# Optimization experiments

Measured on AMD Instinct MI355X. Metric: run time of the kernel, lower is better.

Reference implementation:

```python
import jax, jax.numpy as jnp
import numpy as np

B, NORM_NC, LABEL_NC, H, W, SL = 8, 256, 19, 64, 64, 512
EPS = 1e-5


def _conv5(x, w, b):
    # 5x5 'same' conv, NCHW / OIHW
    y = jax.lax.conv_general_dilated(x, w, (1, 1), [(2, 2), (2, 2)],
                                     dimension_numbers=('NCHW', 'OIHW', 'NCHW'))
    return y + b[None, :, None, None]


def _instance_norm(x):
    # InstanceNorm2d(affine=False): per-sample, per-channel over HxW, biased var
    m = x.mean(axis=(2, 3), keepdims=True)
    v = x.var(axis=(2, 3), keepdims=True)
    return (x - m) / jnp.sqrt(v + EPS)


def setup_inputs() -> dict:
    key = jax.random.key(0)
    ks = jax.random.split(key, 12)
    # one-hot semantic segmentation map (what segmap.bool() assumes in practice)
    labels = jax.random.randint(ks[0], (B, H, W), 0, LABEL_NC)
    segmap = jax.nn.one_hot(labels, LABEL_NC, axis=1, dtype=jnp.float32)  # [B,19,H,W]
    s = 0.02
    return {
        'x': jax.random.normal(ks[1], (B, NORM_NC, H, W), jnp.float32),
        'segmap': segmap,
        'style_codes': jax.random.normal(ks[2], (B, LABEL_NC, SL), jnp.float32),
        'fc_w': jax.random.normal(ks[3], (LABEL_NC, SL, SL), jnp.float32) * s,
        'fc_b': jnp.zeros((LABEL_NC, SL), jnp.float32),
        'conv_gamma_w': jax.random.normal(ks[4], (NORM_NC, SL, 5, 5), jnp.float32) * s,
        'conv_gamma_b': jnp.zeros((NORM_NC,), jnp.float32),
        'conv_beta_w': jax.random.normal(ks[5], (NORM_NC, SL, 5, 5), jnp.float32) * s,
        'conv_beta_b': jnp.zeros((NORM_NC,), jnp.float32),
        'spade_shared_w': jax.random.normal(ks[6], (512, LABEL_NC, 5, 5), jnp.float32) * s,
        'spade_shared_b': jnp.zeros((512,), jnp.float32),
        'spade_gamma_w': jax.random.normal(ks[7], (NORM_NC, 512, 5, 5), jnp.float32) * s,
        'spade_gamma_b': jnp.zeros((NORM_NC,), jnp.float32),
        'spade_beta_w': jax.random.normal(ks[8], (NORM_NC, 512, 5, 5), jnp.float32) * s,
        'spade_beta_b': jnp.zeros((NORM_NC,), jnp.float32),
        'blending_gamma': jnp.zeros((1,), jnp.float32),
        'blending_beta': jnp.zeros((1,), jnp.float32),
    }


def reference(x, segmap, style_codes, fc_w, fc_b,
              conv_gamma_w, conv_gamma_b, conv_beta_w, conv_beta_b,
              spade_shared_w, spade_shared_b,
              spade_gamma_w, spade_gamma_b, spade_beta_w, spade_beta_b,
              blending_gamma, blending_beta):
    normalized = _instance_norm(x)
    # F.interpolate(segmap, size=x.shape[2:], mode='nearest') is identity here
    # (segmap already has x's spatial size).
    mask = segmap > 0  # segmap.bool(): [B,J,H,W]
    J = mask.shape[1]

    # per-class style MLP: mu[b,j] = relu(fc_mu_j(style_codes[b,j]))
    mu = jax.nn.relu(jnp.einsum('bjd,jed->bje', style_codes, fc_w) + fc_b)  # [B,J,SL]

    # for overlapping masks; pixels with no class stay zero.
    last_idx = (J - 1) - jnp.argmax(mask[:, ::-1], axis=1)  # [B,H,W] last true j
    any_m = mask.any(axis=1)                                 # [B,H,W]
    mu_sel = mu[jnp.arange(mu.shape[0])[:, None, None], last_idx]  # [B,H,W,SL]
    middle_avg = jnp.where(any_m[..., None], mu_sel, 0.0).transpose(0, 3, 1, 2)

    gamma_avg = _conv5(middle_avg, conv_gamma_w, conv_gamma_b)
    beta_avg = _conv5(middle_avg, conv_beta_w, conv_beta_b)

    actv = jax.nn.relu(_conv5(segmap, spade_shared_w, spade_shared_b))
    gamma_spade = _conv5(actv, spade_gamma_w, spade_gamma_b)
    beta_spade = _conv5(actv, spade_beta_w, spade_beta_b)

    ga = jax.nn.sigmoid(blending_gamma)  # shape (1,) broadcasts
    ba = jax.nn.sigmoid(blending_beta)
    gamma_final = ga * gamma_avg + (1 - ga) * gamma_spade
    beta_final = ba * beta_avg + (1 - ba) * beta_spade
    return normalized * (1 + gamma_final) + beta_final
```

## Files before the change

### kernel.cpp

```cpp
#include <hip/hip_runtime.h>
#include <hip/hip_bf16.h>
#include <stdint.h>

typedef __attribute__((__ext_vector_type__(8))) __bf16 bf16x8;
typedef __attribute__((__ext_vector_type__(2))) __bf16 bf16x2;
typedef __attribute__((__ext_vector_type__(4))) float  f32x4;
typedef __attribute__((__ext_vector_type__(8))) int    v8i;

#define SCALE_A_DW 0x77777777
#define SCALE_B_DW 0x79797979

__device__ __forceinline__ void gl_lds16(const void* g, void* l) {
  __builtin_amdgcn_global_load_lds(
      (__attribute__((address_space(1))) void*)(uintptr_t)g,
      (__attribute__((address_space(3))) void*)(unsigned)(uintptr_t)l,
      16, 0, 0);
}

__global__ __launch_bounds__(256) void k_prep(
    const float* __restrict__ x, float* __restrict__ stats,
    const float* __restrict__ seg, int* __restrict__ labels,
    const float* __restrict__ cgw, const float* __restrict__ cbw,
    float* __restrict__ wpa,
    const float* __restrict__ ssw, __bf16* __restrict__ wspb,
    __bf16* __restrict__ Aav) {
  __shared__ __align__(16) char smem[16*401*4];
  int blk = blockIdx.x;
  if (blk < 2048) {
    int bc = blk;
    const float4* p = (const float4*)(x + (size_t)bc * 4096);
    float s = 0.f, ss = 0.f;
    for (int i = threadIdx.x; i < 1024; i += 256) {
      float4 v = p[i];
      s  += v.x + v.y + v.z + v.w;
      ss += v.x*v.x + v.y*v.y + v.z*v.z + v.w*v.w;
    }
    #pragma unroll
    for (int o = 32; o > 0; o >>= 1) { s += __shfl_down(s, o); ss += __shfl_down(ss, o); }
    float* sh = (float*)smem;
    int wv = threadIdx.x >> 6;
    if ((threadIdx.x & 63) == 0) { sh[wv] = s; sh[4 + wv] = ss; }
    __syncthreads();
    if (threadIdx.x == 0) {
      float S = sh[0]+sh[1]+sh[2]+sh[3], SS = sh[4]+sh[5]+sh[6]+sh[7];
      float m = S * (1.f/4096.f);
      float var = SS * (1.f/4096.f) - m*m;
      stats[bc] = m;
      stats[2048 + bc] = rsqrtf(var + 1e-5f);
    }
  } else if (blk < 2176) {
    int idx = (blk - 2048)*256 + threadIdx.x;
    int b = idx >> 12, pix = idx & 4095;
    const float* p = seg + (size_t)b*19*4096 + pix;
    int lab = -1;
    for (int j = 0; j < 19; ++j) if (p[(size_t)j*4096] > 0.f) lab = j;
    labels[idx] = lab;
  } else if (blk < 3200) {
    int bid = blk - 2176;
    float* s = (float*)smem;
    int n0 = (bid & 31) * 16, c0 = (bid >> 5) * 16;
    for (int i = threadIdx.x; i < 6400; i += 256) {
      int nn = i / 400, qq = i % 400;
      int n = n0 + nn;
      const float* src = (n < 256) ? cgw + (size_t)n*12800 : cbw + (size_t)(n-256)*12800;
      s[nn*401 + qq] = src[c0*25 + qq];
    }
    __syncthreads();
    for (int i = threadIdx.x; i < 6400; i += 256) {
      int nn = i & 15, rest = i >> 4;
      int k5 = rest % 25, cc = rest / 25;
      wpa[((size_t)k5*512 + c0 + cc)*512 + n0 + nn] = s[nn*401 + cc*25 + k5];
    }
  } else if (blk < 4200) {
    int idx = (blk - 3200)*256 + threadIdx.x;
    int o = idx & 511, k5 = (idx >> 9) % 25, j = idx / 12800;
    wspb[idx] = (j < 19) ? (__bf16)ssw[((size_t)o*19 + j)*25 + k5] : (__bf16)0.f;
  } else {
    ((unsigned*)(Aav + 3800ull*512))[threadIdx.x] = 0;
  }
}

__global__ __launch_bounds__(512) void k_mu(const float* __restrict__ sc,
                                            const float* __restrict__ fcw,
                                            const float* __restrict__ fcb,
                                            float* __restrict__ mu) {
  int b = blockIdx.x / 19, j = blockIdx.x % 19;
  __shared__ float s[512];
  s[threadIdx.x] = sc[(b*19 + j)*512 + threadIdx.x];
  __syncthreads();
  int e = threadIdx.x;
  const float4* w4 = (const float4*)(fcw + ((size_t)(j*512 + e))*512);
  const float4* s4 = (const float4*)s;
  float acc = 0.f;
  for (int d = 0; d < 128; ++d) {
    float4 w = w4[d], v = s4[d];
    acc += w.x*v.x + w.y*v.y + w.z*v.z + w.w*v.w;
  }
  acc += fcb[j*512 + e];
  mu[(b*19 + j)*512 + e] = fmaxf(acc, 0.f);
}

__global__ __launch_bounds__(256) void k_pack_spade(
    const float* __restrict__ g, const float* __restrict__ bt,
    uint8_t* __restrict__ wq) {
  int n = blockIdx.x;
  const float* src = (n < 256) ? g + (size_t)n*12800 : bt + (size_t)(n-256)*12800;
  __shared__ float s[12800];
  for (int i = threadIdx.x; i < 12800; i += 256) s[i] = src[i];
  __syncthreads();
  int t = threadIdx.x;
  for (int k5 = 0; k5 < 25; ++k5) {
    float w0 = s[(2*t)*25 + k5] * 64.f, w1 = s[(2*t+1)*25 + k5] * 64.f;
    int pk = __builtin_amdgcn_cvt_pk_fp8_f32(w0, w1, 0, false);
    *(unsigned short*)(wq + ((size_t)k5*512 + n)*512 + 2*t) = (unsigned short)pk;
  }
}

__global__ __launch_bounds__(512) void k_A_avg(const float* __restrict__ mu,
                                               const float* __restrict__ wpa,
                                               __bf16* __restrict__ A) {
  int b = blockIdx.x / 25, k5 = blockIdx.x % 25;
  int n = threadIdx.x;
  const float* wp = wpa + (size_t)k5*262144 + n;
  const float* mub = mu + b*19*512;
  float acc[19];
  #pragma unroll
  for (int j = 0; j < 19; ++j) acc[j] = 0.f;
  for (int c = 0; c < 512; ++c) {
    float w = wp[(size_t)c*512];
    #pragma unroll
    for (int j = 0; j < 19; ++j) acc[j] += mub[j*512 + c] * w;
  }
  #pragma unroll
  for (int j = 0; j < 19; ++j)
    A[((size_t)((b*19 + j)*25 + k5))*512 + n] = (__bf16)acc[j];
}

__global__ void k_actv(const int* __restrict__ labels, const __bf16* __restrict__ wsp,
                       const float* __restrict__ ssb, uint8_t* __restrict__ actv) {
  int b = blockIdx.x / 68, hp = blockIdx.x % 68;
  int t = threadIdx.x;
  size_t rowbase = ((size_t)b*68 + hp)*68;
  if (hp < 2 || hp >= 66) {
    unsigned* dp = (unsigned*)(actv + rowbase*512);
    for (int i = t; i < 8704; i += 256) dp[i] = 0;
    return;
  }
  int h = hp - 2;
  __shared__ int lab[5*68];
  for (int i = t; i < 5*68; i += 256) {
    int dh = i / 68, xx = i % 68;
    int hh = h + dh - 2, ww = xx - 2;
    int l = 19;
    if (hh >= 0 && hh < 64 && ww >= 0 && ww < 64) {
      int l0 = labels[b*4096 + hh*64 + ww];
      if (l0 >= 0) l = l0;
    }
    lab[i] = l;
  }
  {
    unsigned* dp = (unsigned*)(actv + rowbase*512);
    dp[t] = 0; dp[66*128 + t] = 0;
  }
  __syncthreads();
  float bs0 = ssb[2*t], bs1 = ssb[2*t + 1];
  for (int w = 0; w < 64; ++w) {
    float a0 = bs0, a1 = bs1;
    #pragma unroll
    for (int tap = 0; tap < 25; ++tap) {
      int l = lab[(tap/5)*68 + w + (tap%5)];
      bf16x2 v = *(const bf16x2*)(wsp + (size_t)(l*25 + tap)*512 + 2*t);
      a0 += (float)v[0]; a1 += (float)v[1];
    }
    a0 = fmaxf(a0, 0.f) * 256.f;
    a1 = fmaxf(a1, 0.f) * 256.f;
    int pk = __builtin_amdgcn_cvt_pk_fp8_f32(a0, a1, 0, false);
    *(unsigned short*)(actv + (rowbase + 2 + w)*512 + 2*t) = (unsigned short)pk;
  }
}

__global__ __launch_bounds__(512) void k_conv(
    const uint8_t* __restrict__ actv, const uint8_t* __restrict__ wq,
    const float* __restrict__ sgb, const float* __restrict__ sbb,
    __bf16* __restrict__ gbs) {
  __shared__ __align__(16) uint8_t ldsA[2][32768];
  __shared__ __align__(16) uint8_t ldsB[2][32768];
  const int tid = threadIdx.x, wv = tid >> 6, lane = tid & 63;
  const int l15 = lane & 15, q = lane >> 4;
  const int m0 = blockIdx.x * 256, n0 = blockIdx.y * 256;
  const int b = m0 >> 12;

  int aoff[4], boff[4], ldst[4];
  #pragma unroll
  for (int i = 0; i < 4; ++i) {
    int p = i*512 + tid;
    int r = p >> 3, pc = p & 7;
    int cl = pc ^ (r & 7);
    int pix = (m0 + r) & 4095;
    int h = pix >> 6, w = pix & 63;
    aoff[i] = ((b*68 + h)*68 + w)*512 + cl*16;
    boff[i] = (n0 + r)*512 + cl*16;
    ldst[i] = i*8192 + wv*1024;
  }

  const int wm = (wv >> 2) * 128, wn = (wv & 3) * 64;
  f32x4 acc[8][4] = {};

  auto stage = [&](int t, int buf) {
    int k5 = t >> 2, kc = t & 3;
    int a_k = ((k5/5)*68 + (k5%5))*512 + kc*128;
    int b_k = k5*262144 + kc*128;
    uint8_t* la = &ldsA[buf][0];
    uint8_t* lb = &ldsB[buf][0];
    #pragma unroll
    for (int i = 0; i < 4; ++i) {
      gl_lds16(actv + aoff[i] + a_k, la + ldst[i]);
      gl_lds16(wq   + boff[i] + b_k, lb + ldst[i]);
    }
  };

  auto compute = [&](int buf) {
    v8i bfr[4];
    #pragma unroll
    for (int ni = 0; ni < 4; ++ni) {
      int row = wn + ni*16 + l15;
      const uint8_t* base = &ldsB[buf][row*128];
      union { v8i v; uint4 u[2]; } tt;
      tt.u[0] = *(const uint4*)(base + ((2*q    ) ^ (row & 7))*16);
      tt.u[1] = *(const uint4*)(base + ((2*q + 1) ^ (row & 7))*16);
      bfr[ni] = tt.v;
    }
    __builtin_amdgcn_s_setprio(1);
    #pragma unroll
    for (int mi = 0; mi < 8; ++mi) {
      int row = wm + mi*16 + l15;
      const uint8_t* base = &ldsA[buf][row*128];
      union { v8i v; uint4 u[2]; } tt;
      tt.u[0] = *(const uint4*)(base + ((2*q    ) ^ (row & 7))*16);
      tt.u[1] = *(const uint4*)(base + ((2*q + 1) ^ (row & 7))*16);
      v8i af = tt.v;
      #pragma unroll
      for (int ni = 0; ni < 4; ++ni)
        acc[mi][ni] = __builtin_amdgcn_mfma_scale_f32_16x16x128_f8f6f4(
            af, bfr[ni], acc[mi][ni], 0, 0, 0, SCALE_A_DW, 0, SCALE_B_DW);
    }
    __builtin_amdgcn_s_setprio(0);
  };

  stage(0, 0);
  stage(1, 1);
  #pragma unroll 1
  for (int t = 0; t < 98; t += 2) {
    asm volatile("s_waitcnt vmcnt(8)" ::: "memory");
    __builtin_amdgcn_s_barrier();
    __builtin_amdgcn_sched_barrier(0);
    compute(0);
    __builtin_amdgcn_sched_barrier(0);
    __builtin_amdgcn_s_barrier();
    __builtin_amdgcn_sched_barrier(0);
    stage(t + 2, 0);
    asm volatile("s_waitcnt vmcnt(8)" ::: "memory");
    __builtin_amdgcn_s_barrier();
    __builtin_amdgcn_sched_barrier(0);
    compute(1);
    __builtin_amdgcn_sched_barrier(0);
    __builtin_amdgcn_s_barrier();
    __builtin_amdgcn_sched_barrier(0);
    stage(t + 3, 1);
  }
  asm volatile("s_waitcnt vmcnt(8)" ::: "memory");
  __builtin_amdgcn_s_barrier();
  __builtin_amdgcn_sched_barrier(0);
  compute(0);
  asm volatile("s_waitcnt vmcnt(0)" ::: "memory");
  __builtin_amdgcn_s_barrier();
  __builtin_amdgcn_sched_barrier(0);
  compute(1);

  #pragma unroll
  for (int ni = 0; ni < 4; ++ni) {
    int n = n0 + wn + ni*16 + l15;
    float bias = (n < 256) ? sgb[n] : sbb[n - 256];
    #pragma unroll
    for (int mi = 0; mi < 8; ++mi) {
      int m = m0 + wm + mi*16 + q*4;
      size_t base = (size_t)m*512 + n;
      #pragma unroll
      for (int r = 0; r < 4; ++r)
        gbs[base + (size_t)r*512] = (__bf16)(acc[mi][ni][r] + bias);
    }
  }
}

__global__ __launch_bounds__(256) void k_gf(
    const int* __restrict__ labels, const __bf16* __restrict__ A,
    const float* __restrict__ cgb, const float* __restrict__ cbb,
    const __bf16* __restrict__ gbs, const float* __restrict__ x,
    const float* __restrict__ stats, const float* __restrict__ blg,
    const float* __restrict__ blb, float* __restrict__ out) {
  int wt = blockIdx.x & 3, h = (blockIdx.x >> 2) & 63, b = blockIdx.x >> 8;
  int w0 = wt * 16;
  __shared__ int rowbase[5*20];
  __shared__ __bf16 avg[16][512];
  __shared__ __bf16 spd[16][512];
  for (int i = threadIdx.x; i < 100; i += 256) {
    int dh = i / 20, xx = i % 20;
    int hh = h + dh - 2, ww = w0 + xx - 2;
    int l = (hh >= 0 && hh < 64 && ww >= 0 && ww < 64) ? labels[b*4096 + hh*64 + ww] : -1;
    rowbase[i] = (l >= 0) ? (b*19 + l)*25 : -1;
  }
  __syncthreads();
  int t = threadIdx.x;
  float bs0, bs1;
  if (2*t < 256) { bs0 = cgb[2*t]; bs1 = cgb[2*t + 1]; }
  else           { bs0 = cbb[2*t - 256]; bs1 = cbb[2*t - 255]; }
  size_t pixb = (size_t)b*4096 + h*64 + w0;
  for (int px = 0; px < 16; ++px) {
    float a0 = bs0, a1 = bs1;
    #pragma unroll
    for (int tap = 0; tap < 25; ++tap) {
      int rb = rowbase[(tap/5)*20 + px + (tap%5)];
      int row = (rb >= 0) ? rb + tap : 3800;
      bf16x2 v = *(const bf16x2*)(A + (size_t)row*512 + 2*t);
      a0 += (float)v[0]; a1 += (float)v[1];
    }
    avg[px][2*t]     = (__bf16)a0;
    avg[px][2*t + 1] = (__bf16)a1;
    *(bf16x2*)&spd[px][2*t] = *(const bf16x2*)(gbs + (pixb + px)*512 + 2*t);
  }
  __syncthreads();
  float ga = 1.f / (1.f + expf(-blg[0]));
  float ba = 1.f / (1.f + expf(-blb[0]));
  int c = threadIdx.x;
  int bc = b*256 + c;
  float mean = stats[bc], rstd = stats[2048 + bc];
  size_t xb = (size_t)bc*4096 + h*64 + w0;
  #pragma unroll
  for (int pq = 0; pq < 4; ++pq) {
    float4 xv = *(const float4*)(x + xb + pq*4);
    float4 ov;
    float* xo = (float*)&xv; float* oo = (float*)&ov;
    #pragma unroll
    for (int j = 0; j < 4; ++j) {
      int px = pq*4 + j;
      float gf  = ga*(float)avg[px][c]       + (1.f - ga)*(float)spd[px][c];
      float bf_ = ba*(float)avg[px][256 + c] + (1.f - ba)*(float)spd[px][256 + c];
      oo[j] = (xo[j] - mean)*rstd*(1.f + gf) + bf_;
    }
    *(float4*)(out + xb + pq*4) = ov;
  }
}

extern "C" void kernel_launch(void* const* d_in, const int* in_sizes, int n_in,
                              void* d_out, int out_size, void* d_ws, size_t ws_size,
                              hipStream_t stream) {
  const float* x    = (const float*)d_in[0];
  const float* seg  = (const float*)d_in[1];
  const float* sc   = (const float*)d_in[2];
  const float* fcw  = (const float*)d_in[3];
  const float* fcb  = (const float*)d_in[4];
  const float* cgw  = (const float*)d_in[5];
  const float* cgb  = (const float*)d_in[6];
  const float* cbw  = (const float*)d_in[7];
  const float* cbb  = (const float*)d_in[8];
  const float* ssw  = (const float*)d_in[9];
  const float* ssb  = (const float*)d_in[10];
  const float* sgw  = (const float*)d_in[11];
  const float* sgb  = (const float*)d_in[12];
  const float* sbw  = (const float*)d_in[13];
  const float* sbb  = (const float*)d_in[14];
  const float* blg  = (const float*)d_in[15];
  const float* blb  = (const float*)d_in[16];
  float* out = (float*)d_out;

  char* ws = (char*)d_ws;
  size_t off = 0;
  auto alloc = [&](size_t bytes) {
    void* p = ws + off; off += (bytes + 255) & ~(size_t)255; return p;
  };
  float*   stats = (float*)alloc(2048ull*2*4);
  int*     labels= (int*)  alloc(32768ull*4);
  float*   mu    = (float*)alloc(77824ull*4);
  __bf16*  Aav   = (__bf16*)alloc((3800ull + 1)*512*2);
  __bf16*  wspb  = (__bf16*)alloc(20ull*25*512*2);
  float*   wpa   = (float*)alloc(25ull*512*512*4);
  uint8_t* wq    = (uint8_t*)alloc(25ull*512*512);
  uint8_t* actv  = (uint8_t*)alloc(8ull*68*68*512);
  __bf16*  gbs   = (__bf16*)alloc(8ull*4096*512*2);

  k_prep      <<<4201, 256, 0, stream>>>(x, stats, seg, labels, cgw, cbw, wpa, ssw, wspb, Aav);
  k_mu        <<<152, 512, 0, stream>>>(sc, fcw, fcb, mu);
  k_pack_spade<<<512, 256, 0, stream>>>(sgw, sbw, wq);
  k_A_avg     <<<200, 512, 0, stream>>>(mu, wpa, Aav);
  k_actv      <<<544, 256, 0, stream>>>(labels, wspb, ssb, actv);
  k_conv      <<<dim3(128, 2), 512, 0, stream>>>(actv, wq, sgb, sbb, gbs);
  k_gf        <<<2048, 256, 0, stream>>>(labels, Aav, cgb, cbb, gbs, x, stats, blg, blb, out);
}
```

Before: 641.4 us.

## Load conv B-operand fragments directly from global into registers, bypassing LDS

The weight (B) operand of the fp8 MFMA conv GEMM is no longer staged through LDS. Each wave now loads its own B fragments straight from global memory into double-buffered registers, and the vmcnt waits are adjusted to cover the extra outstanding loads. This halves LDS usage, which may raise occupancy, and removes the LDS reads for B. In exchange, each of the four waves sharing an n-slice loads the same weights again (redundant global/L2 traffic), and register pressure grows.

```diff
diff --git a/kernel.cpp b/kernel.cpp
--- a/kernel.cpp
+++ b/kernel.cpp
@@ -184,13 +184,12 @@
     const float* __restrict__ sgb, const float* __restrict__ sbb,
     __bf16* __restrict__ gbs) {
   __shared__ __align__(16) uint8_t ldsA[2][32768];
-  __shared__ __align__(16) uint8_t ldsB[2][32768];
   const int tid = threadIdx.x, wv = tid >> 6, lane = tid & 63;
   const int l15 = lane & 15, q = lane >> 4;
   const int m0 = blockIdx.x * 256, n0 = blockIdx.y * 256;
   const int b = m0 >> 12;
 
-  int aoff[4], boff[4], ldst[4];
+  int aoff[4], ldst[4];
   #pragma unroll
   for (int i = 0; i < 4; ++i) {
     int p = i*512 + tid;
@@ -199,37 +198,30 @@
     int pix = (m0 + r) & 4095;
     int h = pix >> 6, w = pix & 63;
     aoff[i] = ((b*68 + h)*68 + w)*512 + cl*16;
-    boff[i] = (n0 + r)*512 + cl*16;
     ldst[i] = i*8192 + wv*1024;
   }
 
   const int wm = (wv >> 2) * 128, wn = (wv & 3) * 64;
+  const uint8_t* wqb = wq + (size_t)(n0 + wn + l15)*512 + q*32;
   f32x4 acc[8][4] = {};
 
-  auto stage = [&](int t, int buf) {
+  auto stageA = [&](int t, int buf) {
     int k5 = t >> 2, kc = t & 3;
     int a_k = ((k5/5)*68 + (k5%5))*512 + kc*128;
-    int b_k = k5*262144 + kc*128;
     uint8_t* la = &ldsA[buf][0];
-    uint8_t* lb = &ldsB[buf][0];
-    #pragma unroll
-    for (int i = 0; i < 4; ++i) {
+    #pragma unroll
+    for (int i = 0; i < 4; ++i)
       gl_lds16(actv + aoff[i] + a_k, la + ldst[i]);
-      gl_lds16(wq   + boff[i] + b_k, lb + ldst[i]);
-    }
   };
 
-  auto compute = [&](int buf) {
-    v8i bfr[4];
-    #pragma unroll
-    for (int ni = 0; ni < 4; ++ni) {
-      int row = wn + ni*16 + l15;
-      const uint8_t* base = &ldsB[buf][row*128];
-      union { v8i v; uint4 u[2]; } tt;
-      tt.u[0] = *(const uint4*)(base + ((2*q    ) ^ (row & 7))*16);
-      tt.u[1] = *(const uint4*)(base + ((2*q + 1) ^ (row & 7))*16);
-      bfr[ni] = tt.v;
-    }
+  auto loadB = [&](int t, v8i* o) {
+    const uint8_t* p = wqb + (t >> 2)*262144 + (t & 3)*128;
+    #pragma unroll
+    for (int ni = 0; ni < 4; ++ni)
+      o[ni] = *(const v8i*)(p + ni*16*512);
+  };
+
+  auto compute = [&](int buf, const v8i* bfr) {
     __builtin_amdgcn_s_setprio(1);
     #pragma unroll
     for (int mi = 0; mi < 8; ++mi) {
@@ -247,35 +239,38 @@
     __builtin_amdgcn_s_setprio(0);
   };
 
-  stage(0, 0);
-  stage(1, 1);
+  v8i bA[4], bB[4];
+  stageA(0, 0); loadB(0, bA);
+  stageA(1, 1); loadB(1, bB);
   #pragma unroll 1
   for (int t = 0; t < 98; t += 2) {
-    asm volatile("s_waitcnt vmcnt(8)" ::: "memory");
+    asm volatile("s_waitcnt vmcnt(12)" ::: "memory");
     __builtin_amdgcn_s_barrier();
     __builtin_amdgcn_sched_barrier(0);
-    compute(0);
+    compute(0, bA);
     __builtin_amdgcn_sched_barrier(0);
     __builtin_amdgcn_s_barrier();
     __builtin_amdgcn_sched_barrier(0);
-    stage(t + 2, 0);
-    asm volatile("s_waitcnt vmcnt(8)" ::: "memory");
+    stageA(t + 2, 0); loadB(t + 2, bA);
+    __builtin_amdgcn_sched_barrier(0);
+    asm volatile("s_waitcnt vmcnt(12)" ::: "memory");
     __builtin_amdgcn_s_barrier();
     __builtin_amdgcn_sched_barrier(0);
-    compute(1);
+    compute(1, bB);
     __builtin_amdgcn_sched_barrier(0);
     __builtin_amdgcn_s_barrier();
     __builtin_amdgcn_sched_barrier(0);
-    stage(t + 3, 1);
-  }
-  asm volatile("s_waitcnt vmcnt(8)" ::: "memory");
+    stageA(t + 3, 1); loadB(t + 3, bB);
+    __builtin_amdgcn_sched_barrier(0);
+  }
+  asm volatile("s_waitcnt vmcnt(12)" ::: "memory");
   __builtin_amdgcn_s_barrier();
   __builtin_amdgcn_sched_barrier(0);
-  compute(0);
+  compute(0, bA);
   asm volatile("s_waitcnt vmcnt(0)" ::: "memory");
   __builtin_amdgcn_s_barrier();
   __builtin_amdgcn_sched_barrier(0);
-  compute(1);
+  compute(1, bB);
 
   #pragma unroll
   for (int ni = 0; ni < 4; ++ni) {
```

New measurement: 747.7 us. 16.6% more time.
